# Kernel optimization log

Hardware: AMD Instinct MI355X
Metric: run time of the kernel (lower is better)

## Reference

```python
import jax, jax.numpy as jnp
import numpy as np

MASK_P = 0.15
MASK_LEN = 8
B, H, W, C = 64, 512, 256, 4


def setup_inputs() -> dict:
    key = jax.random.key(0)
    k1, k2, k3, k4, k5 = jax.random.split(key, 5)
    x = jax.random.normal(k1, (B, H, W, C), dtype=jnp.float32)
    time_rand = jax.random.uniform(k2, (B, MASK_LEN, W, C), dtype=jnp.float32)
    freq_rand = jax.random.uniform(k3, (B, H, MASK_LEN, C), dtype=jnp.float32)
    time_starts = jax.random.randint(k4, (B,), 0, H - MASK_LEN + 1, dtype=jnp.int32)
    freq_starts = jax.random.randint(k5, (B,), 0, W - MASK_LEN + 1, dtype=jnp.int32)
    return {"x": x, "time_rand": time_rand, "freq_rand": freq_rand,
            "time_starts": time_starts, "freq_starts": freq_starts}


def _combined_mask(time_rand, freq_rand, time_starts, freq_starts, h, w):
    # Bernoulli masks from uniform draws (cast of comparison, like tf.cast(u < p))
    tmask = jnp.where(time_rand < MASK_P, 1.0, 0.0)   # [B, L, W, C]
    fmask = jnp.where(freq_rand < MASK_P, 1.0, 0.0)   # [B, H, L, C]

    # --- time masking: pad each sample's [L,W,C] strip to height h at start_i,
    # then (faithful to the original broadcast) take product over the batch.
    rel_h = jnp.arange(h)[None, :] - time_starts[:, None]          # [B, H]
    valid_h = (rel_h >= 0) & (rel_h < MASK_LEN)                    # [B, H]
    idx_h = jnp.clip(rel_h, 0, MASK_LEN - 1)[:, :, None, None]    # [B, H, 1, 1]
    padded_t = jnp.take_along_axis(tmask, idx_h, axis=1)           # [B, H, W, C]
    padded_t = jnp.where(valid_h[:, :, None, None], padded_t, 0.0)
    mask_t = jnp.prod(1.0 - padded_t, axis=0)                      # [H, W, C]

    # --- freq masking, same pattern along the width axis.
    rel_w = jnp.arange(w)[None, :] - freq_starts[:, None]          # [B, W]
    valid_w = (rel_w >= 0) & (rel_w < MASK_LEN)                    # [B, W]
    idx_w = jnp.clip(rel_w, 0, MASK_LEN - 1)[:, None, :, None]    # [B, 1, W, 1]
    padded_f = jnp.take_along_axis(fmask, idx_w, axis=2)           # [B, H, W, C]
    padded_f = jnp.where(valid_w[:, None, :, None], padded_f, 0.0)
    mask_f = jnp.prod(1.0 - padded_f, axis=0)                      # [H, W, C]

    return mask_t * mask_f                                         # [H, W, C]


def reference(x, time_rand, freq_rand, time_starts, freq_starts):
    b, h, w, c = x.shape
    mask = _combined_mask(time_rand, freq_rand, time_starts, freq_starts, h, w)
    return x * mask[None]  # same mask broadcast over batch, as in the original
```

## Files before the change

kernel.cpp:

```cpp
#include <hip/hip_runtime.h>

constexpr int B_ = 64, H_ = 512, W_ = 256, C_ = 4, L_ = 8;
constexpr int WC     = W_ * C_;
constexpr int HWC    = H_ * WC;
constexpr int HWC4   = HWC / 4;
constexpr int N_TIME = B_ * L_ * WC;
constexpr int N_FREQ = B_ * H_ * L_ * C_;
constexpr long long N4 = 8388608LL;

typedef float floatx4 __attribute__((ext_vector_type(4)));

__global__ __launch_bounds__(256)
void scatter_mask(const float* __restrict__ trand, const float* __restrict__ frand,
                  const int* __restrict__ tstart, const int* __restrict__ fstart,
                  unsigned char* __restrict__ flags) {
    int tid = blockIdx.x * 256 + threadIdx.x;
    if (tid < N_TIME) {
        if (trand[tid] < 0.15f) {
            int wc = tid & (WC - 1);
            int l  = (tid >> 10) & (L_ - 1);
            int b  = tid >> 13;
            int h  = tstart[b] + l;
            flags[h * WC + wc] = 1;
        }
    } else {
        int j = tid - N_TIME;
        if (frand[j] < 0.15f) {
            int c = j & (C_ - 1);
            int l = (j >> 2) & (L_ - 1);
            int h = (j >> 5) & (H_ - 1);
            int b = j >> 14;
            int w = fstart[b] + l;
            flags[h * WC + w * C_ + c] = 1;
        }
    }
}

__global__ __launch_bounds__(256)
void apply_mask(const floatx4* __restrict__ x4,
                const unsigned int* __restrict__ flag32,
                floatx4* __restrict__ out4) {
    const int base = blockIdx.x * 1024 + threadIdx.x;
    floatx4 a0 = x4[base];
    floatx4 a1 = x4[base + 256];
    floatx4 a2 = x4[base + 512];
    floatx4 a3 = x4[base + 768];
    unsigned f0 = flag32[ base         & (HWC4 - 1)];
    unsigned f1 = flag32[(base +  256) & (HWC4 - 1)];
    unsigned f2 = flag32[(base +  512) & (HWC4 - 1)];
    unsigned f3 = flag32[(base +  768) & (HWC4 - 1)];
    if (f0 & 0xffu) a0.x = 0.f;  if (f0 & 0xff00u) a0.y = 0.f;
    if (f0 & 0xff0000u) a0.z = 0.f;  if (f0 & 0xff000000u) a0.w = 0.f;
    if (f1 & 0xffu) a1.x = 0.f;  if (f1 & 0xff00u) a1.y = 0.f;
    if (f1 & 0xff0000u) a1.z = 0.f;  if (f1 & 0xff000000u) a1.w = 0.f;
    if (f2 & 0xffu) a2.x = 0.f;  if (f2 & 0xff00u) a2.y = 0.f;
    if (f2 & 0xff0000u) a2.z = 0.f;  if (f2 & 0xff000000u) a2.w = 0.f;
    if (f3 & 0xffu) a3.x = 0.f;  if (f3 & 0xff00u) a3.y = 0.f;
    if (f3 & 0xff0000u) a3.z = 0.f;  if (f3 & 0xff000000u) a3.w = 0.f;
    __builtin_nontemporal_store(a0, &out4[base]);
    __builtin_nontemporal_store(a1, &out4[base + 256]);
    __builtin_nontemporal_store(a2, &out4[base + 512]);
    __builtin_nontemporal_store(a3, &out4[base + 768]);
}

constexpr int ROWS = 2, BCH = 8;
__global__ __launch_bounds__(256)
void mask_apply_fused(const float* __restrict__ x, const float* __restrict__ trand,
                      const float* __restrict__ frand, const int* __restrict__ tstart,
                      const int* __restrict__ fstart, float* __restrict__ out) {
    __shared__ int flagw[ROWS * WC / 4];
    __shared__ int ts_s[B_], fs_s[B_];
    unsigned char* flags = (unsigned char*)flagw;
    const int t = threadIdx.x, h0 = blockIdx.x * ROWS, b0 = blockIdx.y * BCH;
    flagw[2 * t] = 0; flagw[2 * t + 1] = 0;
    if (t < B_) { ts_s[t] = tstart[t]; fs_s[t] = fstart[t]; }
    __syncthreads();
    for (int b = 0; b < B_; ++b) {
        int ts = ts_s[b];
#pragma unroll
        for (int r = 0; r < ROWS; ++r) {
            int l = h0 + r - ts;
            if ((unsigned)l < (unsigned)L_) {
                const float* row = trand + (b * L_ + l) * WC;
#pragma unroll
                for (int k = 0; k < 4; ++k)
                    if (row[t * 4 + k] < 0.15f) flags[r * WC + t * 4 + k] = 1;
            }
        }
    }
    {
        int bsub = t >> 5, lane = t & 31, l = lane >> 2, c = lane & 3;
        for (int bb = 0; bb < B_; bb += 8) {
            int b = bb + bsub, fs = fs_s[b];
#pragma unroll
            for (int r = 0; r < ROWS; ++r) {
                float vf = frand[(b * H_ + h0 + r) * (L_ * C_) + l * C_ + c];
                if (vf < 0.15f) flags[r * WC + (fs + l) * C_ + c] = 1;
            }
        }
    }
    __syncthreads();
    const unsigned fw0 = (unsigned)flagw[t], fw1 = (unsigned)flagw[256 + t];
    for (int bi = 0; bi < BCH; ++bi) {
        int base = (b0 + bi) * HWC + h0 * WC;
        float4 v0 = ((const float4*)(x + base))[t];
        float4 v1 = ((const float4*)(x + base + WC))[t];
        if (fw0 & 0xffu)       v0.x = 0.f;
        if (fw0 & 0xff00u)     v0.y = 0.f;
        if (fw0 & 0xff0000u)   v0.z = 0.f;
        if (fw0 & 0xff000000u) v0.w = 0.f;
        if (fw1 & 0xffu)       v1.x = 0.f;
        if (fw1 & 0xff00u)     v1.y = 0.f;
        if (fw1 & 0xff0000u)   v1.z = 0.f;
        if (fw1 & 0xff000000u) v1.w = 0.f;
        ((float4*)(out + base))[t]      = v0;
        ((float4*)(out + base + WC))[t] = v1;
    }
}

extern "C" void kernel_launch(void* const* d_in, const int* in_sizes, int n_in,
                              void* d_out, int out_size, void* d_ws, size_t ws_size,
                              hipStream_t stream) {
    const float* x  = (const float*)d_in[0];
    const float* tr = (const float*)d_in[1];
    const float* fr = (const float*)d_in[2];
    const int*   ts = (const int*)d_in[3];
    const int*   fs = (const int*)d_in[4];
    float* out = (float*)d_out;

    if (ws_size >= (size_t)HWC) {
        unsigned char* flags = (unsigned char*)d_ws;
        (void)hipMemsetAsync(flags, 0, HWC, stream);
        scatter_mask<<<(N_TIME + N_FREQ) / 256, 256, 0, stream>>>(tr, fr, ts, fs, flags);
        apply_mask<<<(int)(N4 / 1024), 256, 0, stream>>>(
            (const floatx4*)x, (const unsigned int*)flags, (floatx4*)out);
    } else {
        dim3 grid(H_ / ROWS, B_ / BCH);
        mask_apply_fused<<<grid, 256, 0, stream>>>(x, tr, fr, ts, fs, out);
    }
}
```

Baseline: 244.4 us.

## Replace memset+scatter+apply pipeline with single fused per-row mask kernel

Removes the workspace path (memset, scatter kernel, apply kernel) and always runs one fused kernel. Each block builds one row's flags in shared memory from the time and frequency random draws, then applies them to 16 batch samples. Loads and stores go through nontemporal builtins. This drops two extra launches and the flag round-trip through global memory, but every block now rebuilds its row's mask, so mask building is repeated 4 times per row.

```diff
diff --git a/kernel.cpp b/kernel.cpp
--- a/kernel.cpp
+++ b/kernel.cpp
@@ -1,120 +1,61 @@
 #include <hip/hip_runtime.h>
 
+
 constexpr int B_ = 64, H_ = 512, W_ = 256, C_ = 4, L_ = 8;
-constexpr int WC     = W_ * C_;
-constexpr int HWC    = H_ * WC;
-constexpr int HWC4   = HWC / 4;
-constexpr int N_TIME = B_ * L_ * WC;
-constexpr int N_FREQ = B_ * H_ * L_ * C_;
-constexpr long long N4 = 8388608LL;
+constexpr int WC  = W_ * C_;
+constexpr int HWC = H_ * WC;
+constexpr int BCH = 16;
 
 typedef float floatx4 __attribute__((ext_vector_type(4)));
 
 __global__ __launch_bounds__(256)
-void scatter_mask(const float* __restrict__ trand, const float* __restrict__ frand,
-                  const int* __restrict__ tstart, const int* __restrict__ fstart,
-                  unsigned char* __restrict__ flags) {
-    int tid = blockIdx.x * 256 + threadIdx.x;
-    if (tid < N_TIME) {
-        if (trand[tid] < 0.15f) {
-            int wc = tid & (WC - 1);
-            int l  = (tid >> 10) & (L_ - 1);
-            int b  = tid >> 13;
-            int h  = tstart[b] + l;
-            flags[h * WC + wc] = 1;
-        }
-    } else {
-        int j = tid - N_TIME;
-        if (frand[j] < 0.15f) {
-            int c = j & (C_ - 1);
-            int l = (j >> 2) & (L_ - 1);
-            int h = (j >> 5) & (H_ - 1);
-            int b = j >> 14;
-            int w = fstart[b] + l;
-            flags[h * WC + w * C_ + c] = 1;
+void fused_row(const float* __restrict__ x, const float* __restrict__ trand,
+               const float* __restrict__ frand, const int* __restrict__ tstart,
+               const int* __restrict__ fstart, float* __restrict__ out) {
+    __shared__ unsigned int flagw[WC / 4];
+    __shared__ int ts_s[B_], fs_s[B_];
+    const int t  = threadIdx.x;
+    const int h  = blockIdx.x;
+    const int b0 = blockIdx.y * BCH;
+
+    flagw[t] = 0u;
+    if (t < B_) { ts_s[t] = tstart[t]; fs_s[t] = fstart[t]; }
+    __syncthreads();
+
+    unsigned char* flags = (unsigned char*)flagw;
+
+    for (int b = 0; b < B_; ++b) {
+        int l = h - ts_s[b];
+        if ((unsigned)l < (unsigned)L_) {
+            const floatx4 v = ((const floatx4*)(trand + (size_t)(b * L_ + l) * WC))[t];
+            if (v.x < 0.15f) flags[t * 4 + 0] = 1;
+            if (v.y < 0.15f) flags[t * 4 + 1] = 1;
+            if (v.z < 0.15f) flags[t * 4 + 2] = 1;
+            if (v.w < 0.15f) flags[t * 4 + 3] = 1;
         }
     }
-}
 
-__global__ __launch_bounds__(256)
-void apply_mask(const floatx4* __restrict__ x4,
-                const unsigned int* __restrict__ flag32,
-                floatx4* __restrict__ out4) {
-    const int base = blockIdx.x * 1024 + threadIdx.x;
-    floatx4 a0 = x4[base];
-    floatx4 a1 = x4[base + 256];
-    floatx4 a2 = x4[base + 512];
-    floatx4 a3 = x4[base + 768];
-    unsigned f0 = flag32[ base         & (HWC4 - 1)];
-    unsigned f1 = flag32[(base +  256) & (HWC4 - 1)];
-    unsigned f2 = flag32[(base +  512) & (HWC4 - 1)];
-    unsigned f3 = flag32[(base +  768) & (HWC4 - 1)];
-    if (f0 & 0xffu) a0.x = 0.f;  if (f0 & 0xff00u) a0.y = 0.f;
-    if (f0 & 0xff0000u) a0.z = 0.f;  if (f0 & 0xff000000u) a0.w = 0.f;
-    if (f1 & 0xffu) a1.x = 0.f;  if (f1 & 0xff00u) a1.y = 0.f;
-    if (f1 & 0xff0000u) a1.z = 0.f;  if (f1 & 0xff000000u) a1.w = 0.f;
-    if (f2 & 0xffu) a2.x = 0.f;  if (f2 & 0xff00u) a2.y = 0.f;
-    if (f2 & 0xff0000u) a2.z = 0.f;  if (f2 & 0xff000000u) a2.w = 0.f;
-    if (f3 & 0xffu) a3.x = 0.f;  if (f3 & 0xff00u) a3.y = 0.f;
-    if (f3 & 0xff0000u) a3.z = 0.f;  if (f3 & 0xff000000u) a3.w = 0.f;
-    __builtin_nontemporal_store(a0, &out4[base]);
-    __builtin_nontemporal_store(a1, &out4[base + 256]);
-    __builtin_nontemporal_store(a2, &out4[base + 512]);
-    __builtin_nontemporal_store(a3, &out4[base + 768]);
-}
-
-constexpr int ROWS = 2, BCH = 8;
-__global__ __launch_bounds__(256)
-void mask_apply_fused(const float* __restrict__ x, const float* __restrict__ trand,
-                      const float* __restrict__ frand, const int* __restrict__ tstart,
-                      const int* __restrict__ fstart, float* __restrict__ out) {
-    __shared__ int flagw[ROWS * WC / 4];
-    __shared__ int ts_s[B_], fs_s[B_];
-    unsigned char* flags = (unsigned char*)flagw;
-    const int t = threadIdx.x, h0 = blockIdx.x * ROWS, b0 = blockIdx.y * BCH;
-    flagw[2 * t] = 0; flagw[2 * t + 1] = 0;
-    if (t < B_) { ts_s[t] = tstart[t]; fs_s[t] = fstart[t]; }
-    __syncthreads();
-    for (int b = 0; b < B_; ++b) {
-        int ts = ts_s[b];
 #pragma unroll
-        for (int r = 0; r < ROWS; ++r) {
-            int l = h0 + r - ts;
-            if ((unsigned)l < (unsigned)L_) {
-                const float* row = trand + (b * L_ + l) * WC;
-#pragma unroll
-                for (int k = 0; k < 4; ++k)
-                    if (row[t * 4 + k] < 0.15f) flags[r * WC + t * 4 + k] = 1;
-            }
-        }
-    }
-    {
-        int bsub = t >> 5, lane = t & 31, l = lane >> 2, c = lane & 3;
-        for (int bb = 0; bb < B_; bb += 8) {
-            int b = bb + bsub, fs = fs_s[b];
-#pragma unroll
-            for (int r = 0; r < ROWS; ++r) {
-                float vf = frand[(b * H_ + h0 + r) * (L_ * C_) + l * C_ + c];
-                if (vf < 0.15f) flags[r * WC + (fs + l) * C_ + c] = 1;
-            }
-        }
+    for (int jj = 0; jj < 8; ++jj) {
+        int j = jj * 256 + t;
+        int b = j >> 5, l = (j >> 2) & 7, c = j & 3;
+        float v = frand[(size_t)(b * H_ + h) * (L_ * C_) + l * C_ + c];
+        if (v < 0.15f) flags[(fs_s[b] + l) * C_ + c] = 1;
     }
     __syncthreads();
-    const unsigned fw0 = (unsigned)flagw[t], fw1 = (unsigned)flagw[256 + t];
+
+    const unsigned fw = flagw[t];
+    const size_t rowoff = (size_t)h * WC;
+
+#pragma unroll 4
     for (int bi = 0; bi < BCH; ++bi) {
-        int base = (b0 + bi) * HWC + h0 * WC;
-        float4 v0 = ((const float4*)(x + base))[t];
-        float4 v1 = ((const float4*)(x + base + WC))[t];
-        if (fw0 & 0xffu)       v0.x = 0.f;
-        if (fw0 & 0xff00u)     v0.y = 0.f;
-        if (fw0 & 0xff0000u)   v0.z = 0.f;
-        if (fw0 & 0xff000000u) v0.w = 0.f;
-        if (fw1 & 0xffu)       v1.x = 0.f;
-        if (fw1 & 0xff00u)     v1.y = 0.f;
-        if (fw1 & 0xff0000u)   v1.z = 0.f;
-        if (fw1 & 0xff000000u) v1.w = 0.f;
-        ((float4*)(out + base))[t]      = v0;
-        ((float4*)(out + base + WC))[t] = v1;
+        const size_t base = (size_t)(b0 + bi) * HWC + rowoff;
+        floatx4 v = __builtin_nontemporal_load((const floatx4*)(x + base) + t);
+        if (fw & 0x000000ffu) v.x = 0.f;
+        if (fw & 0x0000ff00u) v.y = 0.f;
+        if (fw & 0x00ff0000u) v.z = 0.f;
+        if (fw & 0xff000000u) v.w = 0.f;
+        __builtin_nontemporal_store(v, (floatx4*)(out + base) + t);
     }
 }
 
@@ -128,14 +69,6 @@
     const int*   fs = (const int*)d_in[4];
     float* out = (float*)d_out;
 
-    if (ws_size >= (size_t)HWC) {
-        unsigned char* flags = (unsigned char*)d_ws;
-        (void)hipMemsetAsync(flags, 0, HWC, stream);
-        scatter_mask<<<(N_TIME + N_FREQ) / 256, 256, 0, stream>>>(tr, fr, ts, fs, flags);
-        apply_mask<<<(int)(N4 / 1024), 256, 0, stream>>>(
-            (const floatx4*)x, (const unsigned int*)flags, (floatx4*)out);
-    } else {
-        dim3 grid(H_ / ROWS, B_ / BCH);
-        mask_apply_fused<<<grid, 256, 0, stream>>>(x, tr, fr, ts, fs, out);
-    }
+    dim3 grid(H_, B_ / BCH);
+    fused_row<<<grid, 256, 0, stream>>>(x, tr, fr, ts, fs, out);
 }
```

After: 238.4 us. -2.5%, faster.
